# Kernel optimization log

Hardware: AMD Instinct MI355X
Metric: run time of the kernel (lower is better)

## Reference

```python
import jax, jax.numpy as jnp
import numpy as np


def setup_inputs() -> dict:
    key = jax.random.key(0)
    k1, k2, k3 = jax.random.split(key, 3)
    N, M, D, K = 8192, 8192, 512, 128
    x = jax.random.normal(k1, (N, D), dtype=jnp.float32)
    target = jax.random.normal(k2, (M, D), dtype=jnp.float32)
    W = jax.random.normal(k3, (D, K), dtype=jnp.float32) * 0.05
    return {"x": x, "target": target, "W": W}


def reference(x, target, W):
    # phi_Brenier(x): convex potential f(x) = logsumexp(x @ W)  -> [N]
    phi_b = jax.nn.logsumexp(x @ W, axis=-1)
    # phi_Kantorovich = 0.5||x||^2 - phi_Brenier  -> [N]
    x_sq = jnp.sum(x * x, axis=-1)
    phi_k = 0.5 * x_sq - phi_b
    t_sq = jnp.sum(target * target, axis=-1)
    DD = 0.5 * (x_sq[:, None] + t_sq[None, :] - 2.0 * (x @ target.T))
    # C-transform: min over source points  -> [M]
    phi_c = jnp.min(DD - phi_k[:, None], axis=0)
    # Kantorovich dual objective (scalar)
    return jnp.mean(phi_k) + jnp.mean(phi_c)
```

## Files before the change

### kernel.cpp

```cpp
#include <hip/hip_runtime.h>
#include <hip/hip_bf16.h>
#include <stdint.h>

typedef __attribute__((ext_vector_type(8))) short short8;
typedef __attribute__((ext_vector_type(4))) float f32x4;
typedef __attribute__((ext_vector_type(16))) float f32x16;
typedef __attribute__((ext_vector_type(4))) int i32x4;
typedef __attribute__((ext_vector_type(8))) int i32x8;

#define N_PTS 8192
#define M_PTS 8192
#define DIM   512
#define KDIM  128
#define BT    128
#define BKS   32

__device__ __forceinline__ unsigned fenc(float f) {
  unsigned u = __float_as_uint(f);
  return (u & 0x80000000u) ? ~u : (u | 0x80000000u);
}
__device__ __forceinline__ float fdec(unsigned k) {
  unsigned u = (k & 0x80000000u) ? (k ^ 0x80000000u) : ~k;
  return __uint_as_float(u);
}

__device__ __forceinline__ unsigned short f2bf(float f) {
  union { __hip_bfloat16 h; unsigned short u; } c;
  c.h = __float2bfloat16(f);
  return c.u;
}

__device__ __forceinline__ unsigned f2e4m3(float f) {
  unsigned u = __float_as_uint(f);
  unsigned s = (u >> 24) & 0x80;
  unsigned mag = u & 0x7fffffffu;
  unsigned r = mag + 0x0007ffffu + ((mag >> 20) & 1u);
  int e = (int)(r >> 23) - 127;
  if (e < -6) return s;
  unsigned m = (r >> 20) & 7u;
  return s | (unsigned)((e + 7) << 3) | m;
}

__device__ __forceinline__ void async_copy16(const void* g, void* l) {
  __builtin_amdgcn_global_load_lds(
      (const __attribute__((address_space(1))) void*)g,
      (__attribute__((address_space(3))) void*)l, 16, 0, 0);
}

__device__ __forceinline__ int swz_slot(int row, int slot) {
  return slot ^ ((row >> 1) & 3);
}

__device__ __forceinline__ int chunk_key(int row) {
  return ((row >> 1) & 3) ^ ((row >> 3) & 1) ^ (((row >> 4) & 1) << 1);
}

#define BARRIER __builtin_amdgcn_s_barrier()

__global__ __launch_bounds__(256)
void prep_all_kernel(const float* __restrict__ x, const float* __restrict__ tgt,
                     const float* __restrict__ W,
                     unsigned short* __restrict__ Xb, unsigned char* __restrict__ Xf8,
                     unsigned char* __restrict__ TfT, unsigned short* __restrict__ WbT,
                     float* __restrict__ xsq, float* __restrict__ tsq,
                     unsigned* __restrict__ keys) {
  const int bid = blockIdx.x;
  const int tid = threadIdx.x;
  if (bid >= (N_PTS + M_PTS) / 4) {
    const int o = (bid - (N_PTS + M_PTS) / 4) * 256 + tid;
    const int k = o >> 9, d = o & 511;
    WbT[o] = f2bf(W[d * KDIM + k]);
    return;
  }
  const int gw = (bid * 256 + tid) >> 6;
  const int j = tid & 63;
  float s;
  if (gw < N_PTS) {
    const float* src = x + (size_t)gw * DIM + j * 8;
    float4 v0 = *(const float4*)src;
    float4 v1 = *(const float4*)(src + 4);
    s = v0.x * v0.x + v0.y * v0.y + v0.z * v0.z + v0.w * v0.w +
        v1.x * v1.x + v1.y * v1.y + v1.z * v1.z + v1.w * v1.w;
    unsigned short* db = Xb + (size_t)gw * DIM + j * 8;
    ushort4 ob0, ob1;
    ob0.x = f2bf(v0.x); ob0.y = f2bf(v0.y); ob0.z = f2bf(v0.z); ob0.w = f2bf(v0.w);
    ob1.x = f2bf(v1.x); ob1.y = f2bf(v1.y); ob1.z = f2bf(v1.z); ob1.w = f2bf(v1.w);
    *(ushort4*)db = ob0;
    *(ushort4*)(db + 4) = ob1;
    unsigned long long p = (unsigned long long)f2e4m3(v0.x)
        | ((unsigned long long)f2e4m3(v0.y) << 8)
        | ((unsigned long long)f2e4m3(v0.z) << 16)
        | ((unsigned long long)f2e4m3(v0.w) << 24)
        | ((unsigned long long)f2e4m3(v1.x) << 32)
        | ((unsigned long long)f2e4m3(v1.y) << 40)
        | ((unsigned long long)f2e4m3(v1.z) << 48)
        | ((unsigned long long)f2e4m3(v1.w) << 56);
    *(unsigned long long*)(Xf8 + (size_t)gw * DIM + j * 8) = p;
#pragma unroll
    for (int m = 1; m <= 32; m <<= 1) s += __shfl_xor(s, m);
    if (j == 0) xsq[gw] = s;
  } else {
    const int tr = gw - N_PTS;
    const float* src = tgt + (size_t)tr * DIM + j * 8;
    float4 v0 = *(const float4*)src;
    float4 v1 = *(const float4*)(src + 4);
    s = v0.x * v0.x + v0.y * v0.y + v0.z * v0.z + v0.w * v0.w +
        v1.x * v1.x + v1.y * v1.y + v1.z * v1.z + v1.w * v1.w;
    unsigned long long p = (unsigned long long)f2e4m3(v0.x)
        | ((unsigned long long)f2e4m3(v0.y) << 8)
        | ((unsigned long long)f2e4m3(v0.z) << 16)
        | ((unsigned long long)f2e4m3(v0.w) << 24)
        | ((unsigned long long)f2e4m3(v1.x) << 32)
        | ((unsigned long long)f2e4m3(v1.y) << 40)
        | ((unsigned long long)f2e4m3(v1.z) << 48)
        | ((unsigned long long)f2e4m3(v1.w) << 56);
    *(unsigned long long*)(TfT + ((size_t)(j >> 3) * M_PTS + tr) * 64 + (j & 7) * 8) = p;
#pragma unroll
    for (int m = 1; m <= 32; m <<= 1) s += __shfl_xor(s, m);
    if (j == 0) { tsq[tr] = s; keys[tr] = 0xFFFFFFFFu; }
  }
}

__global__ __launch_bounds__(256)
void phi_b_kernel(const short* __restrict__ Xb, const short* __restrict__ WbT,
                  float* __restrict__ phi_b) {
  __shared__ __align__(16) short As[BT * BKS];
  __shared__ __align__(16) short Bs[BT * BKS];
  __shared__ __align__(16) float lg[128][136];

  const int tid = threadIdx.x;
  const int wave = tid >> 6, lane = tid & 63;
  const int n0 = blockIdx.x * BT;
  const int srow = tid >> 2;
  const int sk8 = swz_slot(srow, tid & 3) * 8;
  const int wr = wave >> 1, wc = wave & 1;
  const int fr = lane & 15, g = lane >> 4;

  f32x4 acc[4][4] = {};
  for (int kt = 0; kt < DIM / BKS; ++kt) {
    const int k0 = kt * BKS;
    async_copy16(Xb + (size_t)(n0 + srow) * DIM + k0 + sk8, &As[wave * 512]);
    async_copy16(Xb + (size_t)(n0 + srow + 64) * DIM + k0 + sk8, &As[2048 + wave * 512]);
    async_copy16(WbT + (size_t)srow * DIM + k0 + sk8, &Bs[wave * 512]);
    async_copy16(WbT + (size_t)(srow + 64) * DIM + k0 + sk8, &Bs[2048 + wave * 512]);
    __syncthreads();
    short8 a[4], b[4];
#pragma unroll
    for (int i = 0; i < 4; ++i) {
      const int R = wr * 64 + i * 16 + fr;
      a[i] = *(const short8*)&As[R * BKS + swz_slot(R, g) * 8];
    }
#pragma unroll
    for (int j = 0; j < 4; ++j) {
      const int R = wc * 64 + j * 16 + fr;
      b[j] = *(const short8*)&Bs[R * BKS + swz_slot(R, g) * 8];
    }
#pragma unroll
    for (int i = 0; i < 4; ++i)
#pragma unroll
      for (int j = 0; j < 4; ++j)
        acc[i][j] = __builtin_amdgcn_mfma_f32_16x16x32_bf16(a[i], b[j], acc[i][j], 0, 0, 0);
    __syncthreads();
  }

  const int rq = g * 4;
#pragma unroll
  for (int i = 0; i < 4; ++i)
#pragma unroll
    for (int j = 0; j < 4; ++j)
#pragma unroll
      for (int q = 0; q < 4; ++q)
        lg[wr * 64 + i * 16 + rq + q][wc * 64 + j * 16 + fr] = acc[i][j][q];
  __syncthreads();

  const int row = tid >> 1, half = tid & 1;
  const float4* lr = (const float4*)(&lg[row][half * 64]);
  float mx = -3.4e38f;
#pragma unroll
  for (int c = 0; c < 16; ++c) {
    float4 v = lr[c];
    mx = fmaxf(mx, fmaxf(fmaxf(v.x, v.y), fmaxf(v.z, v.w)));
  }
  mx = fmaxf(mx, __shfl_xor(mx, 1));
  float s = 0.f;
#pragma unroll
  for (int c = 0; c < 16; ++c) {
    float4 v = lr[c];
    s += __expf(v.x - mx) + __expf(v.y - mx) + __expf(v.z - mx) + __expf(v.w - mx);
  }
  s += __shfl_xor(s, 1);
  if (half == 0) phi_b[n0 + row] = mx + logf(s);
}

__device__ __forceinline__ void stgA(const unsigned char* __restrict__ mat,
                                     int rowbase, int kbyte,
                                     unsigned char* dst, int tid) {
  const int r = tid >> 2, d = tid & 3;
  async_copy16(mat + (size_t)(rowbase + r) * DIM + kbyte + ((d ^ chunk_key(r)) << 4),
               dst + (tid >> 6) * 1024);
}

__device__ __forceinline__ i32x8 ld2x16(const unsigned char* p0, const unsigned char* p1) {
  i32x4 lo = *(const i32x4*)p0;
  i32x4 hi = *(const i32x4*)p1;
  return __builtin_shufflevector(lo, hi, 0, 1, 2, 3, 4, 5, 6, 7);
}

__device__ __forceinline__ f32x16 mfma_mx(i32x8 a, i32x8 b, f32x16 c) {
  return __builtin_amdgcn_mfma_scale_f32_32x32x64_f8f6f4(a, b, c, 0, 0,
                                                         0, 0x7F, 0, 0x7F);
}

template <int VMC, bool STG, bool LDB, bool BAR>
__device__ __forceinline__ void ktile(const unsigned char* Abuf, unsigned char* Sbuf,
                                      const unsigned char* __restrict__ Xf,
                                      const unsigned char* __restrict__ Bnx,
                                      int n0, int kstage, int tid, int aoff,
                                      i32x8 (&fb)[2], i32x8 (&fbn)[2],
                                      f32x16 (&acc)[4][2]) {
  i32x8 fa[4];
#pragma unroll
  for (int i = 0; i < 4; ++i)
    fa[i] = ld2x16(Abuf + aoff + i * 2048, Abuf + ((aoff + i * 2048) ^ 16));
  if (LDB) {
    fbn[0] = ld2x16(Bnx, Bnx + 16);
    fbn[1] = ld2x16(Bnx + 2048, Bnx + 2048 + 16);
  }
  if (STG) {
    stgA(Xf, n0, kstage, Sbuf, tid);
    stgA(Xf, n0 + 128, kstage, Sbuf + 8192, tid);
  }
  __builtin_amdgcn_s_setprio(1);
#pragma unroll
  for (int i = 0; i < 4; ++i) acc[i][0] = mfma_mx(fa[i], fb[0], acc[i][0]);
#pragma unroll
  for (int i = 0; i < 4; ++i) acc[i][1] = mfma_mx(fa[i], fb[1], acc[i][1]);
  __builtin_amdgcn_s_setprio(0);
  if (VMC == 6) asm volatile("s_waitcnt vmcnt(6)" ::: "memory");
  else if (VMC == 4) asm volatile("s_waitcnt vmcnt(4)" ::: "memory");
  else if (VMC == 0) asm volatile("s_waitcnt vmcnt(0)" ::: "memory");
  if (BAR) BARRIER;
}

__global__ __launch_bounds__(512, 2)
void gemm_min_kernel(const unsigned char* __restrict__ Xf, const unsigned char* __restrict__ TfT,
                     const float* __restrict__ phi_b, unsigned* __restrict__ keys) {
  __shared__ __align__(16) unsigned char lds8[49152];

  const int tid = threadIdx.x;
  const int wave = tid >> 6, lane = tid & 63;
  const int wm = wave >> 2, wn = wave & 3;
  const int fr5 = lane & 31, h = lane >> 5;

  const int bid = blockIdx.x;
  const int xcd = bid & 7, idx = bid >> 3;
  const int nt = (xcd >> 1) * 8 + (idx >> 4);
  const int mt = (xcd & 1) * 16 + (idx & 15);
  const int n0 = nt * 256, m0 = mt * 256;

  const int key = chunk_key(fr5);
  const int aoff = (wm * 128 + fr5) * 64 + (((h << 1) ^ key) << 4);

  const unsigned char* Bb = TfT + ((size_t)(m0 + wn * 64 + fr5)) * 64 + h * 32;
#define BK_T(kt) (Bb + (size_t)(kt) * (M_PTS * 64))

  unsigned char* B0 = lds8;
  unsigned char* B1 = lds8 + 16384;
  unsigned char* B2 = lds8 + 32768;

  stgA(Xf, n0, 0, B0, tid);       stgA(Xf, n0 + 128, 0, B0 + 8192, tid);
  stgA(Xf, n0, 64, B1, tid);      stgA(Xf, n0 + 128, 64, B1 + 8192, tid);
  asm volatile("s_waitcnt vmcnt(0)" ::: "memory");
  BARRIER;

  i32x8 fbA[2], fbB[2];
  fbA[0] = ld2x16(BK_T(0), BK_T(0) + 16);
  fbA[1] = ld2x16(BK_T(0) + 2048, BK_T(0) + 2048 + 16);

  f32x16 acc[4][2] = {};
  ktile<6, true, true, true>(B0, B2, Xf, BK_T(1), n0, 128, tid, aoff, fbA, fbB, acc);
  ktile<6, true, true, true>(B1, B0, Xf, BK_T(2), n0, 192, tid, aoff, fbB, fbA, acc);
  ktile<6, true, true, true>(B2, B1, Xf, BK_T(3), n0, 256, tid, aoff, fbA, fbB, acc);
  ktile<6, true, true, true>(B0, B2, Xf, BK_T(4), n0, 320, tid, aoff, fbB, fbA, acc);
  ktile<6, true, true, true>(B1, B0, Xf, BK_T(5), n0, 384, tid, aoff, fbA, fbB, acc);
  ktile<6, true, true, true>(B2, B1, Xf, BK_T(6), n0, 448, tid, aoff, fbB, fbA, acc);
  ktile<4, false, true, true>(B0, B2, Xf, BK_T(7), n0, 0, tid, aoff, fbA, fbB, acc);
  ktile<-1, false, false, false>(B1, B2, Xf, BK_T(7), n0, 0, tid, aoff, fbB, fbA, acc);

  float mv0 = 3.4e38f, mv1 = 3.4e38f;
#pragma unroll
  for (int i = 0; i < 4; ++i) {
    float pb[16];
#pragma unroll
    for (int q = 0; q < 16; ++q)
      pb[q] = phi_b[n0 + wm * 128 + i * 32 + (q & 3) + 8 * (q >> 2) + 4 * h];
#pragma unroll
    for (int q = 0; q < 16; ++q) {
      mv0 = fminf(mv0, pb[q] - acc[i][0][q]);
      mv1 = fminf(mv1, pb[q] - acc[i][1][q]);
    }
  }
  mv0 = fminf(mv0, __shfl_xor(mv0, 32));
  mv1 = fminf(mv1, __shfl_xor(mv1, 32));
  if (h == 0) {
    atomicMin(&keys[m0 + wn * 64 + fr5], fenc(mv0));
    atomicMin(&keys[m0 + wn * 64 + 32 + fr5], fenc(mv1));
  }
#undef BK_T
}

__global__ __launch_bounds__(256)
void partial_kernel(const float* __restrict__ xsq, const float* __restrict__ phi_b,
                    const float* __restrict__ tsq, const unsigned* __restrict__ keys,
                    double* __restrict__ partials) {
  const int b = blockIdx.x, t = threadIdx.x;
  double s;
  if (b < 32) {
    const int n = b * 256 + t;
    s = 0.5 * (double)xsq[n] - (double)phi_b[n];
  } else {
    const int m = (b - 32) * 256 + t;
    s = 0.5 * (double)tsq[m] + (double)fdec(keys[m]);
  }
  const int lane = t & 63, wv = t >> 6;
#pragma unroll
  for (int k = 1; k <= 32; k <<= 1) s += __shfl_xor(s, k);
  __shared__ double ps[4];
  if (lane == 0) ps[wv] = s;
  __syncthreads();
  if (t == 0) partials[b] = ps[0] + ps[1] + ps[2] + ps[3];
}

__global__ __launch_bounds__(64)
void final_kernel(const double* __restrict__ partials, float* __restrict__ out) {
  if (threadIdx.x == 0) {
    double a = 0.0, c = 0.0;
#pragma unroll
    for (int i = 0; i < 32; ++i) a += partials[i];
#pragma unroll
    for (int i = 32; i < 64; ++i) c += partials[i];
    out[0] = (float)(a / N_PTS + c / M_PTS);
  }
}

extern "C" void kernel_launch(void* const* d_in, const int* in_sizes, int n_in,
                              void* d_out, int out_size, void* d_ws, size_t ws_size,
                              hipStream_t stream) {
  const float* x = (const float*)d_in[0];
  const float* tgt = (const float*)d_in[1];
  const float* W = (const float*)d_in[2];

  char* ws = (char*)d_ws;
  const size_t XB_BYTES = (size_t)N_PTS * DIM * 2;
  const size_t XF_BYTES = (size_t)N_PTS * DIM;
  const size_t TF_BYTES = (size_t)M_PTS * DIM;
  const size_t WT_BYTES = (size_t)KDIM * DIM * 2;
  unsigned short* Xb = (unsigned short*)ws;
  unsigned char* Xf8 = (unsigned char*)(ws + XB_BYTES);
  unsigned char* TfT = (unsigned char*)(ws + XB_BYTES + XF_BYTES);
  unsigned short* WbT = (unsigned short*)(ws + XB_BYTES + XF_BYTES + TF_BYTES);
  float* phi_b = (float*)(ws + XB_BYTES + XF_BYTES + TF_BYTES + WT_BYTES);
  float* xsq = phi_b + N_PTS;
  float* tsq = xsq + N_PTS;
  unsigned* keys = (unsigned*)(tsq + M_PTS);
  double* partials = (double*)(keys + M_PTS + 64);

  const int prep_blocks = (N_PTS + M_PTS) / 4 + (KDIM * DIM) / 256;
  prep_all_kernel<<<prep_blocks, 256, 0, stream>>>(x, tgt, W, Xb, Xf8, TfT, WbT,
                                                   xsq, tsq, keys);
  phi_b_kernel<<<N_PTS / BT, 256, 0, stream>>>((const short*)Xb, (const short*)WbT, phi_b);
  gemm_min_kernel<<<(N_PTS / 256) * (M_PTS / 256), 512, 0, stream>>>(Xf8, TfT, phi_b, keys);
  partial_kernel<<<64, 256, 0, stream>>>(xsq, phi_b, tsq, keys, partials);
  final_kernel<<<1, 64, 0, stream>>>(partials, (float*)d_out);
}
```

Before: 69.57 us.

## Drop LDS staging in fp8 GEMM; load both operands directly from k-tiled global layout

The x fp8 copy is now written in the same k-tiled transposed layout as the target, so each wave can load MFMA fragments for both operands straight from global memory. The LDS triple buffer, async copies, waitcnt and barrier pipeline are removed. The wave grid changes from 2x4 to 4x2, with each wave computing a 64x128 tile. This removes LDS traffic and barrier synchronisation, but A fragments are now re-read from global or L2 by several waves and there is no explicit prefetch to hide load latency.

```diff
diff --git a/kernel.cpp b/kernel.cpp
--- a/kernel.cpp
+++ b/kernel.cpp
@@ -51,16 +51,10 @@
   return slot ^ ((row >> 1) & 3);
 }
 
-__device__ __forceinline__ int chunk_key(int row) {
-  return ((row >> 1) & 3) ^ ((row >> 3) & 1) ^ (((row >> 4) & 1) << 1);
-}
-
-#define BARRIER __builtin_amdgcn_s_barrier()
-
 __global__ __launch_bounds__(256)
 void prep_all_kernel(const float* __restrict__ x, const float* __restrict__ tgt,
                      const float* __restrict__ W,
-                     unsigned short* __restrict__ Xb, unsigned char* __restrict__ Xf8,
+                     unsigned short* __restrict__ Xb, unsigned char* __restrict__ XfT,
                      unsigned char* __restrict__ TfT, unsigned short* __restrict__ WbT,
                      float* __restrict__ xsq, float* __restrict__ tsq,
                      unsigned* __restrict__ keys) {
@@ -95,7 +89,7 @@
         | ((unsigned long long)f2e4m3(v1.y) << 40)
         | ((unsigned long long)f2e4m3(v1.z) << 48)
         | ((unsigned long long)f2e4m3(v1.w) << 56);
-    *(unsigned long long*)(Xf8 + (size_t)gw * DIM + j * 8) = p;
+    *(unsigned long long*)(XfT + ((size_t)(j >> 3) * N_PTS + gw) * 64 + (j & 7) * 8) = p;
 #pragma unroll
     for (int m = 1; m <= 32; m <<= 1) s += __shfl_xor(s, m);
     if (j == 0) xsq[gw] = s;
@@ -192,14 +186,6 @@
   if (half == 0) phi_b[n0 + row] = mx + logf(s);
 }
 
-__device__ __forceinline__ void stgA(const unsigned char* __restrict__ mat,
-                                     int rowbase, int kbyte,
-                                     unsigned char* dst, int tid) {
-  const int r = tid >> 2, d = tid & 3;
-  async_copy16(mat + (size_t)(rowbase + r) * DIM + kbyte + ((d ^ chunk_key(r)) << 4),
-               dst + (tid >> 6) * 1024);
-}
-
 __device__ __forceinline__ i32x8 ld2x16(const unsigned char* p0, const unsigned char* p1) {
   i32x4 lo = *(const i32x4*)p0;
   i32x4 hi = *(const i32x4*)p1;
@@ -211,45 +197,12 @@
                                                          0, 0x7F, 0, 0x7F);
 }
 
-template <int VMC, bool STG, bool LDB, bool BAR>
-__device__ __forceinline__ void ktile(const unsigned char* Abuf, unsigned char* Sbuf,
-                                      const unsigned char* __restrict__ Xf,
-                                      const unsigned char* __restrict__ Bnx,
-                                      int n0, int kstage, int tid, int aoff,
-                                      i32x8 (&fb)[2], i32x8 (&fbn)[2],
-                                      f32x16 (&acc)[4][2]) {
-  i32x8 fa[4];
-#pragma unroll
-  for (int i = 0; i < 4; ++i)
-    fa[i] = ld2x16(Abuf + aoff + i * 2048, Abuf + ((aoff + i * 2048) ^ 16));
-  if (LDB) {
-    fbn[0] = ld2x16(Bnx, Bnx + 16);
-    fbn[1] = ld2x16(Bnx + 2048, Bnx + 2048 + 16);
-  }
-  if (STG) {
-    stgA(Xf, n0, kstage, Sbuf, tid);
-    stgA(Xf, n0 + 128, kstage, Sbuf + 8192, tid);
-  }
-  __builtin_amdgcn_s_setprio(1);
-#pragma unroll
-  for (int i = 0; i < 4; ++i) acc[i][0] = mfma_mx(fa[i], fb[0], acc[i][0]);
-#pragma unroll
-  for (int i = 0; i < 4; ++i) acc[i][1] = mfma_mx(fa[i], fb[1], acc[i][1]);
-  __builtin_amdgcn_s_setprio(0);
-  if (VMC == 6) asm volatile("s_waitcnt vmcnt(6)" ::: "memory");
-  else if (VMC == 4) asm volatile("s_waitcnt vmcnt(4)" ::: "memory");
-  else if (VMC == 0) asm volatile("s_waitcnt vmcnt(0)" ::: "memory");
-  if (BAR) BARRIER;
-}
-
 __global__ __launch_bounds__(512, 2)
-void gemm_min_kernel(const unsigned char* __restrict__ Xf, const unsigned char* __restrict__ TfT,
+void gemm_min_kernel(const unsigned char* __restrict__ XfT, const unsigned char* __restrict__ TfT,
                      const float* __restrict__ phi_b, unsigned* __restrict__ keys) {
-  __shared__ __align__(16) unsigned char lds8[49152];
-
   const int tid = threadIdx.x;
   const int wave = tid >> 6, lane = tid & 63;
-  const int wm = wave >> 2, wn = wave & 3;
+  const int wm = wave >> 1, wn = wave & 1;
   const int fr5 = lane & 31, h = lane >> 5;
 
   const int bid = blockIdx.x;
@@ -258,55 +211,51 @@
   const int mt = (xcd & 1) * 16 + (idx & 15);
   const int n0 = nt * 256, m0 = mt * 256;
 
-  const int key = chunk_key(fr5);
-  const int aoff = (wm * 128 + fr5) * 64 + (((h << 1) ^ key) << 4);
-
-  const unsigned char* Bb = TfT + ((size_t)(m0 + wn * 64 + fr5)) * 64 + h * 32;
-#define BK_T(kt) (Bb + (size_t)(kt) * (M_PTS * 64))
-
-  unsigned char* B0 = lds8;
-  unsigned char* B1 = lds8 + 16384;
-  unsigned char* B2 = lds8 + 32768;
-
-  stgA(Xf, n0, 0, B0, tid);       stgA(Xf, n0 + 128, 0, B0 + 8192, tid);
-  stgA(Xf, n0, 64, B1, tid);      stgA(Xf, n0 + 128, 64, B1 + 8192, tid);
-  asm volatile("s_waitcnt vmcnt(0)" ::: "memory");
-  BARRIER;
-
-  i32x8 fbA[2], fbB[2];
-  fbA[0] = ld2x16(BK_T(0), BK_T(0) + 16);
-  fbA[1] = ld2x16(BK_T(0) + 2048, BK_T(0) + 2048 + 16);
-
-  f32x16 acc[4][2] = {};
-  ktile<6, true, true, true>(B0, B2, Xf, BK_T(1), n0, 128, tid, aoff, fbA, fbB, acc);
-  ktile<6, true, true, true>(B1, B0, Xf, BK_T(2), n0, 192, tid, aoff, fbB, fbA, acc);
-  ktile<6, true, true, true>(B2, B1, Xf, BK_T(3), n0, 256, tid, aoff, fbA, fbB, acc);
-  ktile<6, true, true, true>(B0, B2, Xf, BK_T(4), n0, 320, tid, aoff, fbB, fbA, acc);
-  ktile<6, true, true, true>(B1, B0, Xf, BK_T(5), n0, 384, tid, aoff, fbA, fbB, acc);
-  ktile<6, true, true, true>(B2, B1, Xf, BK_T(6), n0, 448, tid, aoff, fbB, fbA, acc);
-  ktile<4, false, true, true>(B0, B2, Xf, BK_T(7), n0, 0, tid, aoff, fbA, fbB, acc);
-  ktile<-1, false, false, false>(B1, B2, Xf, BK_T(7), n0, 0, tid, aoff, fbB, fbA, acc);
-
-  float mv0 = 3.4e38f, mv1 = 3.4e38f;
-#pragma unroll
-  for (int i = 0; i < 4; ++i) {
-    float pb[16];
+  const unsigned char* Ab = XfT + ((size_t)(n0 + wm * 64 + fr5)) * 64 + h * 32;
+  const unsigned char* Bb = TfT + ((size_t)(m0 + wn * 128 + fr5)) * 64 + h * 32;
+  const size_t KT = (size_t)N_PTS * 64;
+
+  f32x16 acc[2][4] = {};
+#pragma unroll
+  for (int kt = 0; kt < 8; ++kt) {
+    i32x8 fa[2], fb[4];
+#pragma unroll
+    for (int i = 0; i < 2; ++i) {
+      const unsigned char* p = Ab + kt * KT + i * 2048;
+      fa[i] = ld2x16(p, p + 16);
+    }
+#pragma unroll
+    for (int j = 0; j < 4; ++j) {
+      const unsigned char* p = Bb + kt * KT + j * 2048;
+      fb[j] = ld2x16(p, p + 16);
+    }
+#pragma unroll
+    for (int i = 0; i < 2; ++i)
+#pragma unroll
+      for (int j = 0; j < 4; ++j)
+        acc[i][j] = mfma_mx(fa[i], fb[j], acc[i][j]);
+  }
+
+  float pb[2][16];
+#pragma unroll
+  for (int i = 0; i < 2; ++i)
 #pragma unroll
     for (int q = 0; q < 16; ++q)
-      pb[q] = phi_b[n0 + wm * 128 + i * 32 + (q & 3) + 8 * (q >> 2) + 4 * h];
-#pragma unroll
-    for (int q = 0; q < 16; ++q) {
-      mv0 = fminf(mv0, pb[q] - acc[i][0][q]);
-      mv1 = fminf(mv1, pb[q] - acc[i][1][q]);
-    }
-  }
-  mv0 = fminf(mv0, __shfl_xor(mv0, 32));
-  mv1 = fminf(mv1, __shfl_xor(mv1, 32));
-  if (h == 0) {
-    atomicMin(&keys[m0 + wn * 64 + fr5], fenc(mv0));
-    atomicMin(&keys[m0 + wn * 64 + 32 + fr5], fenc(mv1));
-  }
-#undef BK_T
+      pb[i][q] = phi_b[n0 + wm * 64 + i * 32 + (q & 3) + 8 * (q >> 2) + 4 * h];
+
+  float mv[4] = {3.4e38f, 3.4e38f, 3.4e38f, 3.4e38f};
+#pragma unroll
+  for (int i = 0; i < 2; ++i)
+#pragma unroll
+    for (int j = 0; j < 4; ++j)
+#pragma unroll
+      for (int q = 0; q < 16; ++q)
+        mv[j] = fminf(mv[j], pb[i][q] - acc[i][j][q]);
+#pragma unroll
+  for (int j = 0; j < 4; ++j) {
+    float v = fminf(mv[j], __shfl_xor(mv[j], 32));
+    if (h == 0) atomicMin(&keys[m0 + wn * 128 + j * 32 + fr5], fenc(v));
+  }
 }
 
 __global__ __launch_bounds__(256)
@@ -356,7 +305,7 @@
   const size_t TF_BYTES = (size_t)M_PTS * DIM;
   const size_t WT_BYTES = (size_t)KDIM * DIM * 2;
   unsigned short* Xb = (unsigned short*)ws;
-  unsigned char* Xf8 = (unsigned char*)(ws + XB_BYTES);
+  unsigned char* XfT = (unsigned char*)(ws + XB_BYTES);
   unsigned char* TfT = (unsigned char*)(ws + XB_BYTES + XF_BYTES);
   unsigned short* WbT = (unsigned short*)(ws + XB_BYTES + XF_BYTES + TF_BYTES);
   float* phi_b = (float*)(ws + XB_BYTES + XF_BYTES + TF_BYTES + WT_BYTES);
@@ -366,10 +315,10 @@
   double* partials = (double*)(keys + M_PTS + 64);
 
   const int prep_blocks = (N_PTS + M_PTS) / 4 + (KDIM * DIM) / 256;
-  prep_all_kernel<<<prep_blocks, 256, 0, stream>>>(x, tgt, W, Xb, Xf8, TfT, WbT,
+  prep_all_kernel<<<prep_blocks, 256, 0, stream>>>(x, tgt, W, Xb, XfT, TfT, WbT,
                                                    xsq, tsq, keys);
   phi_b_kernel<<<N_PTS / BT, 256, 0, stream>>>((const short*)Xb, (const short*)WbT, phi_b);
-  gemm_min_kernel<<<(N_PTS / 256) * (M_PTS / 256), 512, 0, stream>>>(Xf8, TfT, phi_b, keys);
+  gemm_min_kernel<<<(N_PTS / 256) * (M_PTS / 256), 512, 0, stream>>>(XfT, TfT, phi_b, keys);
   partial_kernel<<<64, 256, 0, stream>>>(xsq, phi_b, tsq, keys, partials);
   final_kernel<<<1, 64, 0, stream>>>(partials, (float*)d_out);
 }
```

After: 84.70 us. 21.8% more time.
